# Kernel tuning notes

Hardware: AMD Instinct MI355X
Metric: run time of the kernel (lower is better)

The kernel has to match this reference:

```python
import jax, jax.numpy as jnp
import numpy as np

BATCH, IN_DIM, LATENT, K = 16384, 768, 12288, 32

def setup_inputs() -> dict:
    key = jax.random.key(0)
    k1, k2, k3 = jax.random.split(key, 3)
    # kaiming-uniform-style scale for encoder/decoder weights
    enc_bound = float(np.sqrt(6.0 / IN_DIM))
    dec_bound = float(np.sqrt(6.0 / LATENT))
    x = jax.random.normal(k1, (BATCH, IN_DIM), dtype=jnp.float32)
    enc_w = jax.random.uniform(k2, (LATENT, IN_DIM), dtype=jnp.float32, minval=-enc_bound, maxval=enc_bound)
    enc_b = jnp.zeros((LATENT,), dtype=jnp.float32)
    dec_w = jax.random.uniform(k3, (IN_DIM, LATENT), dtype=jnp.float32, minval=-dec_bound, maxval=dec_bound)
    dec_b = jnp.zeros((IN_DIM,), dtype=jnp.float32)
    return {"x": x, "enc_w": enc_w, "enc_b": enc_b, "dec_w": dec_w, "dec_b": dec_b, "k": K}

def reference(x, enc_w, enc_b, dec_w, dec_b, k):
    # encode: z = x @ W_e^T + b_e            [B, LATENT]
    z = jnp.einsum('bi,li->bl', x, enc_w) + enc_b
    # top-k threshold: kth largest value per row, then shifted relu
    vals, _ = jax.lax.top_k(z, k)
    thresh = vals[:, -1:]                     # [B, 1]
    z_sparse = jax.nn.relu(z - thresh)
    # decode: dense GEMM over all latent columns (as in original module)
    x_recon = jnp.einsum('bl,il->bi', z_sparse, dec_w) + dec_b
    return (x_recon, z_sparse)
```

## Files before the change

kernel.cpp:

```cpp
#include <hip/hip_runtime.h>

#define M_DIM 16384
#define K_DIM 768
#define N_DIM 12288
#define TOPK  32

typedef float f32x4 __attribute__((ext_vector_type(4)));
typedef short s16x8 __attribute__((ext_vector_type(8)));

__device__ __forceinline__ unsigned f2u(float f) {
  union { float f; unsigned u; } v; v.f = f; return v.u;
}
__device__ __forceinline__ float u2f(unsigned u) {
  union { unsigned u; float f; } v; v.u = u; return v.f;
}
__device__ __forceinline__ unsigned fkey(float f) {
  const unsigned u = f2u(f);
  return u ^ (unsigned)(((int)u >> 31) | 0x80000000);
}
__device__ __forceinline__ float kinv(unsigned k) {
  return u2f((k & 0x80000000u) ? (k ^ 0x80000000u) : ~k);
}

__device__ __forceinline__ unsigned short bf16_rne(float f) {
  unsigned u = f2u(f);
  return (unsigned short)((u + 0x7FFFu + ((u >> 16) & 1u)) >> 16);
}

__global__ __launch_bounds__(256) void split_bf16_planes(
    const float* __restrict__ src, unsigned short* __restrict__ hi,
    unsigned short* __restrict__ lo, int n4)
{
  const int stride = (int)(gridDim.x * blockDim.x);
  for (int i = (int)(blockIdx.x * blockDim.x + threadIdx.x); i < n4; i += stride) {
    const float4 v = ((const float4*)src)[i];
    ushort4 h, l;
    h.x = bf16_rne(v.x); h.y = bf16_rne(v.y); h.z = bf16_rne(v.z); h.w = bf16_rne(v.w);
    l.x = bf16_rne(v.x - u2f((unsigned)h.x << 16));
    l.y = bf16_rne(v.y - u2f((unsigned)h.y << 16));
    l.z = bf16_rne(v.z - u2f((unsigned)h.z << 16));
    l.w = bf16_rne(v.w - u2f((unsigned)h.w << 16));
    ((ushort4*)hi)[i] = h;
    ((ushort4*)lo)[i] = l;
  }
}

__device__ __forceinline__ void mfma16(f32x4& d, s16x8 a, s16x8 b) {
  asm("v_mfma_f32_16x16x32_bf16 %0, %1, %2, %0" : "+v"(d) : "v"(a), "v"(b));
}

#define GL16(g, l) __builtin_amdgcn_global_load_lds(                      \
    (const __attribute__((address_space(1))) void*)(g),                   \
    (__attribute__((address_space(3))) void*)(l), 16, 0, 0)

__global__ __launch_bounds__(256, 2) void TopKSparseAutoencoder_51917564674099_kernel(
    const unsigned short* __restrict__ Ahi, const unsigned short* __restrict__ Alo,
    const unsigned short* __restrict__ Bhi, const unsigned short* __restrict__ Blo,
    const float* __restrict__ bias, float* __restrict__ Z)
{
  __shared__ unsigned short lds[4][128][32];

  const int t    = (int)threadIdx.x;
  const int wid  = t >> 6;
  const int lane = t & 63;

  const int bid  = (int)(blockIdx.y * gridDim.x + blockIdx.x);
  const int bswz = (bid & 7) * (12288 / 8) + (bid >> 3);
  const int n0   = (bswz % 96) * 128;
  const int m0   = (bswz / 96) * 128;

  const int rr  = lane >> 2;
  const int kq  = lane & 3;
  const int rt0 = wid * 32 + rr;
  const int rt1 = rt0 + 16;
  const int kc0 = (kq ^ ((rt0 >> 1) & 3)) * 8;
  const int kc1 = (kq ^ ((rt1 >> 1) & 3)) * 8;
  const size_t offA0 = (size_t)(m0 + rt0) * K_DIM + kc0;
  const size_t offA1 = (size_t)(m0 + rt1) * K_DIM + kc1;
  const size_t offB0 = (size_t)(n0 + rt0) * K_DIM + kc0;
  const size_t offB1 = (size_t)(n0 + rt1) * K_DIM + kc1;

  const int wm = (wid >> 1) * 64;
  const int wn = (wid & 1) * 64;
  const int lr = lane & 15;
  const int lc = lane >> 4;

  f32x4 acc[4][4];
#pragma unroll
  for (int i = 0; i < 4; ++i)
#pragma unroll
    for (int j = 0; j < 4; ++j) acc[i][j] = (f32x4){0.f, 0.f, 0.f, 0.f};

  for (int k0 = 0; k0 < K_DIM; k0 += 32) {
    GL16(Ahi + offA0 + k0, &lds[0][wid * 32][0]);
    GL16(Ahi + offA1 + k0, &lds[0][wid * 32 + 16][0]);
    GL16(Alo + offA0 + k0, &lds[1][wid * 32][0]);
    GL16(Alo + offA1 + k0, &lds[1][wid * 32 + 16][0]);
    GL16(Bhi + offB0 + k0, &lds[2][wid * 32][0]);
    GL16(Bhi + offB1 + k0, &lds[2][wid * 32 + 16][0]);
    GL16(Blo + offB0 + k0, &lds[3][wid * 32][0]);
    GL16(Blo + offB1 + k0, &lds[3][wid * 32 + 16][0]);
    __syncthreads();

    s16x8 ah[4], al[4], bh[4], bl[4];
#pragma unroll
    for (int i = 0; i < 4; ++i) {
      const int r = wm + i * 16 + lr;
      const int p = (lc ^ ((r >> 1) & 3)) * 8;
      ah[i] = *(const s16x8*)&lds[0][r][p];
      al[i] = *(const s16x8*)&lds[1][r][p];
    }
#pragma unroll
    for (int j = 0; j < 4; ++j) {
      const int r = wn + j * 16 + lr;
      const int p = (lc ^ ((r >> 1) & 3)) * 8;
      bh[j] = *(const s16x8*)&lds[2][r][p];
      bl[j] = *(const s16x8*)&lds[3][r][p];
    }
#pragma unroll
    for (int i = 0; i < 4; ++i)
#pragma unroll
      for (int j = 0; j < 4; ++j) {
        mfma16(acc[i][j], ah[i], bh[j]);
        mfma16(acc[i][j], ah[i], bl[j]);
        mfma16(acc[i][j], al[i], bh[j]);
      }
    __syncthreads();
  }

  asm volatile("s_nop 7\n\ts_nop 7" :::);

#pragma unroll
  for (int j = 0; j < 4; ++j) {
    const int col = n0 + wn + j * 16 + lr;
    const float bb = bias[col];
#pragma unroll
    for (int i = 0; i < 4; ++i) {
      const int r0 = m0 + wm + i * 16 + lc * 4;
#pragma unroll
      for (int q = 0; q < 4; ++q)
        Z[(size_t)(r0 + q) * N_DIM + col] = acc[i][j][q] + bb;
    }
  }
}

__global__ void enc_gemm_f32_fb(
    const float* A, const float* B, const float* bias, float* Z)
{
  __shared__ float As[32][132];
  __shared__ float Bs[32][132];

  const int tx = (int)threadIdx.x;
  const int ty = (int)threadIdx.y;
  const int t  = ty * 16 + tx;
  const int n0 = (int)blockIdx.x * 128;
  const int m0 = (int)blockIdx.y * 128;
  const int r = t >> 1;
  const int h = (t & 1) * 16;

  float c[8][8];
#pragma unroll
  for (int i = 0; i < 8; ++i)
#pragma unroll
    for (int j = 0; j < 8; ++j) c[i][j] = 0.0f;

  for (int k0 = 0; k0 < K_DIM; k0 += 32) {
    const float* pa = A + (size_t)(m0 + r) * K_DIM + k0 + h;
    const float* pb = B + (size_t)(n0 + r) * K_DIM + k0 + h;
    float fa[16], fb[16];
#pragma unroll
    for (int j = 0; j < 16; ++j) fa[j] = pa[j];
#pragma unroll
    for (int j = 0; j < 16; ++j) fb[j] = pb[j];
#pragma unroll
    for (int j = 0; j < 16; ++j) As[h + j][r] = fa[j];
#pragma unroll
    for (int j = 0; j < 16; ++j) Bs[h + j][r] = fb[j];
    __syncthreads();

    for (int kk = 0; kk < 32; ++kk) {
      float av[8], bv[8];
#pragma unroll
      for (int i = 0; i < 8; ++i) av[i] = As[kk][ty * 8 + i];
#pragma unroll
      for (int j = 0; j < 8; ++j) bv[j] = Bs[kk][tx * 8 + j];
#pragma unroll
      for (int i = 0; i < 8; ++i)
#pragma unroll
        for (int j = 0; j < 8; ++j) c[i][j] += av[i] * bv[j];
    }
    __syncthreads();
  }

#pragma unroll
  for (int j = 0; j < 8; ++j) {
    const int col = n0 + tx * 8 + j;
    const float bb = bias[col];
#pragma unroll
    for (int i = 0; i < 8; ++i)
      Z[(size_t)(m0 + ty * 8 + i) * N_DIM + col] = c[i][j] + bb;
  }
}

__global__ void transpose_decw(const float* W, float* WT)
{
  __shared__ float tile[32][33];
  const int bx = (int)blockIdx.x;
  const int by = (int)blockIdx.y;
  const int tx = (int)threadIdx.x;
  const int ty = (int)threadIdx.y;
#pragma unroll
  for (int j = 0; j < 32; j += 8)
    tile[ty + j][tx] = W[(size_t)(by * 32 + ty + j) * N_DIM + bx * 32 + tx];
  __syncthreads();
#pragma unroll
  for (int j = 0; j < 32; j += 8)
    WT[(size_t)(bx * 32 + ty + j) * K_DIM + by * 32 + tx] = tile[tx][ty + j];
}

__device__ __forceinline__ void full_round(
    const uint4* zk, unsigned red[][2][4], int t, int lane, int wid, int r,
    unsigned& lo, unsigned long long& w)
{
  w >>= 2;
  const unsigned wu = (unsigned)w;
  const unsigned m1 = lo + wu, m2 = lo + 2u * wu, m3 = lo + 3u * wu;
  unsigned c1 = 0, c2 = 0, c3 = 0;
#pragma unroll
  for (int j = 0; j < 12; ++j) {
    const uint4 k = zk[t + 256 * j];
    c1 += (k.x >= m1) + (k.y >= m1) + (k.z >= m1) + (k.w >= m1);
    c2 += (k.x >= m2) + (k.y >= m2) + (k.z >= m2) + (k.w >= m2);
    c3 += (k.x >= m3) + (k.y >= m3) + (k.z >= m3) + (k.w >= m3);
  }
  unsigned p = c1 | (c2 << 16), q = c3;
  p += __shfl_down(p, 32); q += __shfl_down(q, 32);
  p += __shfl_down(p, 16); q += __shfl_down(q, 16);
  p += __shfl_down(p, 8);  q += __shfl_down(q, 8);
  p += __shfl_down(p, 4);  q += __shfl_down(q, 4);
  p += __shfl_down(p, 2);  q += __shfl_down(q, 2);
  p += __shfl_down(p, 1);  q += __shfl_down(q, 1);
  const int par = r & 1;
  if (lane == 0) { red[par][0][wid] = p; red[par][1][wid] = q; }
  __syncthreads();
  const unsigned P = red[par][0][0] + red[par][0][1] + red[par][0][2] + red[par][0][3];
  const unsigned Q = red[par][1][0] + red[par][1][1] + red[par][1][2] + red[par][1][3];
  if (Q >= (unsigned)TOPK)                lo = m3;
  else if ((P >> 16) >= (unsigned)TOPK)   lo = m2;
  else if ((P & 0xFFFFu) >= (unsigned)TOPK) lo = m1;
}

__global__ __launch_bounds__(256, 3) void topk_select_decode(
    float* Z,
    const float* __restrict__ WT,
    const float* __restrict__ DW,
    const float* __restrict__ db,
    float* __restrict__ XR,
    int use_wt)
{
  __shared__ uint4 zkey4[N_DIM / 4];
  __shared__ unsigned red[2][2][4];
  __shared__ unsigned cand[256];
  __shared__ unsigned s_T;
  __shared__ int s_cc;
  __shared__ int s_nnz;
  __shared__ int   s_col[TOPK];
  __shared__ float s_val[TOPK];

  const int row  = (int)blockIdx.x;
  const int t    = (int)threadIdx.x;
  const int lane = t & 63;
  const int wid  = t >> 6;

  float4* zv = (float4*)(Z + (size_t)row * N_DIM);

#pragma unroll
  for (int j = 0; j < 12; ++j) {
    const float4 v = zv[t + 256 * j];
    uint4 k;
    k.x = fkey(v.x); k.y = fkey(v.y); k.z = fkey(v.z); k.w = fkey(v.w);
    zkey4[t + 256 * j] = k;
  }
  if (t == 0) { s_nnz = 0; s_cc = 0; }
  if (t < TOPK) { s_col[t] = 0; s_val[t] = 0.0f; }
  __syncthreads();

  unsigned lo = 0;
  unsigned long long w = 1ULL << 32;
  for (int r = 0; r < 8; ++r)
    full_round(zkey4, red, t, lane, wid, r, lo, w);

#pragma unroll
  for (int j = 0; j < 12; ++j) {
    const uint4 k = zkey4[t + 256 * j];
    if (k.x >= lo) { int p = atomicAdd(&s_cc, 1); if (p < 256) cand[p] = k.x; }
    if (k.y >= lo) { int p = atomicAdd(&s_cc, 1); if (p < 256) cand[p] = k.y; }
    if (k.z >= lo) { int p = atomicAdd(&s_cc, 1); if (p < 256) cand[p] = k.z; }
    if (k.w >= lo) { int p = atomicAdd(&s_cc, 1); if (p < 256) cand[p] = k.w; }
  }
  __syncthreads();
  const int cc = s_cc;

  if (cc <= 256) {
    if (wid == 0) {
      const unsigned k0 = (lane       < cc) ? cand[lane]       : 0u;
      const unsigned k1 = (lane + 64  < cc) ? cand[lane + 64]  : 0u;
      const unsigned k2 = (lane + 128 < cc) ? cand[lane + 128] : 0u;
      const unsigned k3 = (lane + 192 < cc) ? cand[lane + 192] : 0u;
      for (int r = 8; r < 16; ++r) {
        w >>= 2;
        const unsigned wu = (unsigned)w;
        const unsigned m1 = lo + wu, m2 = lo + 2u * wu, m3 = lo + 3u * wu;
        unsigned c1 = (k0 >= m1) + (k1 >= m1) + (k2 >= m1) + (k3 >= m1);
        unsigned c2 = (k0 >= m2) + (k1 >= m2) + (k2 >= m2) + (k3 >= m2);
        unsigned c3 = (k0 >= m3) + (k1 >= m3) + (k2 >= m3) + (k3 >= m3);
        unsigned p = c1 | (c2 << 16), q = c3;
        p += __shfl_down(p, 32); q += __shfl_down(q, 32);
        p += __shfl_down(p, 16); q += __shfl_down(q, 16);
        p += __shfl_down(p, 8);  q += __shfl_down(q, 8);
        p += __shfl_down(p, 4);  q += __shfl_down(q, 4);
        p += __shfl_down(p, 2);  q += __shfl_down(q, 2);
        p += __shfl_down(p, 1);  q += __shfl_down(q, 1);
        p = __shfl(p, 0); q = __shfl(q, 0);
        if (q >= (unsigned)TOPK)                  lo = m3;
        else if ((p >> 16) >= (unsigned)TOPK)     lo = m2;
        else if ((p & 0xFFFFu) >= (unsigned)TOPK) lo = m1;
      }
      if (lane == 0) s_T = lo;
    }
  } else {
    for (int r = 8; r < 16; ++r)
      full_round(zkey4, red, t, lane, wid, r, lo, w);
    if (t == 0) s_T = lo;
  }
  __syncthreads();
  const unsigned T = s_T;
  const float thresh = kinv(T);

#define COMP(KF, OFS, OF) {                                                   \
      float v = 0.0f;                                                         \
      if (KF > T) {                                                           \
        v = kinv(KF) - thresh;                                                \
        const int p = atomicAdd(&s_nnz, 1);                                   \
        if (p < TOPK) { s_col[p] = base + OFS; s_val[p] = v; }                \
      }                                                                       \
      o.OF = v; }
#pragma unroll
  for (int j = 0; j < 12; ++j) {
    const uint4 k = zkey4[t + 256 * j];
    const int base = (t + 256 * j) * 4;
    float4 o;
    COMP(k.x, 0, x)
    COMP(k.y, 1, y)
    COMP(k.z, 2, z)
    COMP(k.w, 3, w)
    zv[t + 256 * j] = o;
  }
#undef COMP
  __syncthreads();

  float a0 = 0.0f, a1 = 0.0f, a2 = 0.0f;
  if (use_wt) {
#pragma unroll 8
    for (int j = 0; j < TOPK; ++j) {
      const float v = s_val[j];
      const float* wp = WT + (size_t)s_col[j] * K_DIM;
      a0 += v * wp[t];
      a1 += v * wp[t + 256];
      a2 += v * wp[t + 512];
    }
  } else {
#pragma unroll 8
    for (int j = 0; j < TOPK; ++j) {
      const float v = s_val[j];
      const int col = s_col[j];
      a0 += v * DW[(size_t)(t)       * N_DIM + col];
      a1 += v * DW[(size_t)(t + 256) * N_DIM + col];
      a2 += v * DW[(size_t)(t + 512) * N_DIM + col];
    }
  }
  float* xr = XR + (size_t)row * K_DIM;
  xr[t]       = a0 + db[t];
  xr[t + 256] = a1 + db[t + 256];
  xr[t + 512] = a2 + db[t + 512];
}

extern "C" void kernel_launch(void* const* d_in, const int* in_sizes, int n_in,
                              void* d_out, int out_size, void* d_ws, size_t ws_size,
                              hipStream_t stream)
{
  (void)in_sizes; (void)n_in; (void)out_size;

  const float* x     = (const float*)d_in[0];
  const float* enc_w = (const float*)d_in[1];
  const float* enc_b = (const float*)d_in[2];
  const float* dec_w = (const float*)d_in[3];
  const float* dec_b = (const float*)d_in[4];

  float* out     = (float*)d_out;
  float* x_recon = out;
  float* z_sp    = out + (size_t)M_DIM * K_DIM;

  const size_t WT_BYTES = (size_t)N_DIM * K_DIM * sizeof(float);
  const size_t XPLANE   = (size_t)M_DIM * K_DIM * sizeof(unsigned short);
  const size_t WPLANE   = (size_t)N_DIM * K_DIM * sizeof(unsigned short);
  const size_t FULL     = WT_BYTES + 2 * XPLANE + 2 * WPLANE;

  char* ws = (char*)d_ws;
  const int use_wt   = (ws_size >= WT_BYTES) ? 1 : 0;
  const int use_mfma = (ws_size >= FULL) ? 1 : 0;

  float*          WT  = (float*)ws;
  unsigned short* xhi = (unsigned short*)(ws + WT_BYTES);
  unsigned short* xlo = (unsigned short*)(ws + WT_BYTES + XPLANE);
  unsigned short* whi = (unsigned short*)(ws + WT_BYTES + 2 * XPLANE);
  unsigned short* wlo = (unsigned short*)(ws + WT_BYTES + 2 * XPLANE + WPLANE);

  if (use_wt) {
    dim3 tb(32, 8);
    dim3 tg(N_DIM / 32, K_DIM / 32);
    transpose_decw<<<tg, tb, 0, stream>>>(dec_w, WT);
  }

  if (use_mfma) {
    split_bf16_planes<<<1024, 256, 0, stream>>>(x, xhi, xlo, M_DIM * K_DIM / 4);
    split_bf16_planes<<<1024, 256, 0, stream>>>(enc_w, whi, wlo, N_DIM * K_DIM / 4);
    dim3 tg(N_DIM / 128, M_DIM / 128);
    TopKSparseAutoencoder_51917564674099_kernel<<<tg, 256, 0, stream>>>(
        xhi, xlo, whi, wlo, enc_b, z_sp);
  } else {
    dim3 tb(16, 16);
    dim3 tg(N_DIM / 128, M_DIM / 128);
    enc_gemm_f32_fb<<<tg, tb, 0, stream>>>(x, enc_w, enc_b, z_sp);
  }

  topk_select_decode<<<M_DIM, 256, 0, stream>>>(z_sp, WT, dec_w, dec_b, x_recon, use_wt);
}
```

Measured before the change: 2.410 ms.

## Emit per-chunk row maxima from encoder GEMM to prune top-k candidate search

The encoder GEMM epilogue now reduces each 128-column tile to per-row maxima and writes them to a workspace array. A new decode kernel first finds a lower bound from those 96 chunk maxima (the 32nd largest chunk max), gathers candidates above it into a small LDS list, and runs the radix select on that list instead of the full row. It also writes zeros with the other waves and scatters the sparse values back. The transpose and bf16 split kernels are merged into one prep launch. This is meant to cut the full-row select passes and launch overhead, at the cost of extra epilogue shuffles, an LDS barrier in the GEMM, and more workspace, which could disable the new path if the workspace is too small.

```diff
diff --git a/kernel.cpp b/kernel.cpp
--- a/kernel.cpp
+++ b/kernel.cpp
@@ -4,6 +4,7 @@
 #define K_DIM 768
 #define N_DIM 12288
 #define TOPK  32
+#define NCHUNK (N_DIM / 128)
 
 typedef float f32x4 __attribute__((ext_vector_type(4)));
 typedef short s16x8 __attribute__((ext_vector_type(8)));
@@ -21,18 +22,47 @@
 __device__ __forceinline__ float kinv(unsigned k) {
   return u2f((k & 0x80000000u) ? (k ^ 0x80000000u) : ~k);
 }
-
 __device__ __forceinline__ unsigned short bf16_rne(float f) {
   unsigned u = f2u(f);
   return (unsigned short)((u + 0x7FFFu + ((u >> 16) & 1u)) >> 16);
 }
 
-__global__ __launch_bounds__(256) void split_bf16_planes(
-    const float* __restrict__ src, unsigned short* __restrict__ hi,
-    unsigned short* __restrict__ lo, int n4)
+__global__ __launch_bounds__(256) void TopKSparseAutoencoder_51917564674099_prep(
+    const float* __restrict__ x, const float* __restrict__ w,
+    const float* __restrict__ dw,
+    unsigned short* __restrict__ xhi, unsigned short* __restrict__ xlo,
+    unsigned short* __restrict__ whi, unsigned short* __restrict__ wlo,
+    float* __restrict__ WT, int do_t, int do_s)
 {
-  const int stride = (int)(gridDim.x * blockDim.x);
-  for (int i = (int)(blockIdx.x * blockDim.x + threadIdx.x); i < n4; i += stride) {
+  __shared__ float tile[32][33];
+  const int b = (int)blockIdx.x;
+  const int t = (int)threadIdx.x;
+
+  if (b < 9216) {
+    if (!do_t) return;
+    const int bx = b % (N_DIM / 32);
+    const int by = b / (N_DIM / 32);
+    const int tx = t & 31, ty = t >> 5;
+#pragma unroll
+    for (int j = 0; j < 32; j += 8)
+      tile[ty + j][tx] = dw[(size_t)(by * 32 + ty + j) * N_DIM + bx * 32 + tx];
+    __syncthreads();
+#pragma unroll
+    for (int j = 0; j < 32; j += 8)
+      WT[(size_t)(bx * 32 + ty + j) * K_DIM + by * 32 + tx] = tile[tx][ty + j];
+    return;
+  }
+  if (!do_s) return;
+
+  const float* src; unsigned short* dh; unsigned short* dl; int i, stride, n4;
+  if (b < 9216 + 1024) {
+    src = x; dh = xhi; dl = xlo;
+    i = (b - 9216) * 256 + t; stride = 1024 * 256; n4 = M_DIM * K_DIM / 4;
+  } else {
+    src = w; dh = whi; dl = wlo;
+    i = (b - 10240) * 256 + t; stride = 512 * 256; n4 = N_DIM * K_DIM / 4;
+  }
+  for (; i < n4; i += stride) {
     const float4 v = ((const float4*)src)[i];
     ushort4 h, l;
     h.x = bf16_rne(v.x); h.y = bf16_rne(v.y); h.z = bf16_rne(v.z); h.w = bf16_rne(v.w);
@@ -40,8 +70,8 @@
     l.y = bf16_rne(v.y - u2f((unsigned)h.y << 16));
     l.z = bf16_rne(v.z - u2f((unsigned)h.z << 16));
     l.w = bf16_rne(v.w - u2f((unsigned)h.w << 16));
-    ((ushort4*)hi)[i] = h;
-    ((ushort4*)lo)[i] = l;
+    ((ushort4*)dh)[i] = h;
+    ((ushort4*)dl)[i] = l;
   }
 }
 
@@ -56,9 +86,11 @@
 __global__ __launch_bounds__(256, 2) void TopKSparseAutoencoder_51917564674099_kernel(
     const unsigned short* __restrict__ Ahi, const unsigned short* __restrict__ Alo,
     const unsigned short* __restrict__ Bhi, const unsigned short* __restrict__ Blo,
-    const float* __restrict__ bias, float* __restrict__ Z)
+    const float* __restrict__ bias, float* __restrict__ Z,
+    float* __restrict__ cmax, int do_cmax)
 {
   __shared__ unsigned short lds[4][128][32];
+  __shared__ float cmx[128][2];
 
   const int t    = (int)threadIdx.x;
   const int wid  = t >> 6;
@@ -130,6 +162,12 @@
 
   asm volatile("s_nop 7\n\ts_nop 7" :::);
 
+  float mx[4][4];
+#pragma unroll
+  for (int i = 0; i < 4; ++i)
+#pragma unroll
+    for (int q = 0; q < 4; ++q) mx[i][q] = -3.4e38f;
+
 #pragma unroll
   for (int j = 0; j < 4; ++j) {
     const int col = n0 + wn + j * 16 + lr;
@@ -138,9 +176,32 @@
     for (int i = 0; i < 4; ++i) {
       const int r0 = m0 + wm + i * 16 + lc * 4;
 #pragma unroll
-      for (int q = 0; q < 4; ++q)
-        Z[(size_t)(r0 + q) * N_DIM + col] = acc[i][j][q] + bb;
-    }
+      for (int q = 0; q < 4; ++q) {
+        const float val = acc[i][j][q] + bb;
+        Z[(size_t)(r0 + q) * N_DIM + col] = val;
+        mx[i][q] = fmaxf(mx[i][q], val);
+      }
+    }
+  }
+
+  if (do_cmax) {
+#pragma unroll
+    for (int s = 1; s < 16; s <<= 1)
+#pragma unroll
+      for (int i = 0; i < 4; ++i)
+#pragma unroll
+        for (int q = 0; q < 4; ++q)
+          mx[i][q] = fmaxf(mx[i][q], __shfl_xor(mx[i][q], s));
+    if (lr == 0) {
+#pragma unroll
+      for (int i = 0; i < 4; ++i)
+#pragma unroll
+        for (int q = 0; q < 4; ++q)
+          cmx[wm + i * 16 + lc * 4 + q][wid & 1] = mx[i][q];
+    }
+    __syncthreads();
+    if (t < 128)
+      cmax[(size_t)(m0 + t) * NCHUNK + (n0 >> 7)] = fmaxf(cmx[t][0], cmx[t][1]);
   }
 }
 
@@ -202,23 +263,179 @@
   }
 }
 
-__global__ void transpose_decw(const float* W, float* WT)
+__global__ __launch_bounds__(256, 4) void TopKSparseAutoencoder_51917564674099_zdecode(
+    float* Z, const float* __restrict__ CMAX, const float* __restrict__ WT,
+    const float* __restrict__ db, float* __restrict__ XR)
 {
-  __shared__ float tile[32][33];
-  const int bx = (int)blockIdx.x;
-  const int by = (int)blockIdx.y;
-  const int tx = (int)threadIdx.x;
-  const int ty = (int)threadIdx.y;
-#pragma unroll
-  for (int j = 0; j < 32; j += 8)
-    tile[ty + j][tx] = W[(size_t)(by * 32 + ty + j) * N_DIM + bx * 32 + tx];
+  __shared__ unsigned candk[512];
+  __shared__ int      candi[512];
+  __shared__ unsigned red[2][2][4];
+  __shared__ unsigned s_B;
+  __shared__ int s_cc, s_nnz;
+  __shared__ int   s_col[TOPK];
+  __shared__ float s_val[TOPK];
+
+  const int row  = (int)blockIdx.x;
+  const int t    = (int)threadIdx.x;
+  const int lane = t & 63;
+  const int wid  = t >> 6;
+
+  if (t == 0) { s_cc = 0; s_nnz = 0; }
+  if (t < TOPK) { s_col[t] = 0; s_val[t] = 0.0f; }
+
+  if (wid == 0) {
+    const unsigned kA = fkey(CMAX[(size_t)row * NCHUNK + lane]);
+    const unsigned kB = (lane < NCHUNK - 64) ? fkey(CMAX[(size_t)row * NCHUNK + 64 + lane]) : 0u;
+    unsigned lo = 0;
+    unsigned long long w = 1ULL << 32;
+    for (int r = 0; r < 8; ++r) {
+      w >>= 2;
+      const unsigned wu = (unsigned)w;
+      const unsigned m1 = lo + wu, m2 = lo + 2u * wu, m3 = lo + 3u * wu;
+      unsigned p = (unsigned)((kA >= m1) + (kB >= m1)) |
+                   ((unsigned)((kA >= m2) + (kB >= m2)) << 16);
+      unsigned q = (unsigned)((kA >= m3) + (kB >= m3));
+      p += __shfl_down(p, 32); q += __shfl_down(q, 32);
+      p += __shfl_down(p, 16); q += __shfl_down(q, 16);
+      p += __shfl_down(p, 8);  q += __shfl_down(q, 8);
+      p += __shfl_down(p, 4);  q += __shfl_down(q, 4);
+      p += __shfl_down(p, 2);  q += __shfl_down(q, 2);
+      p += __shfl_down(p, 1);  q += __shfl_down(q, 1);
+      p = __shfl(p, 0); q = __shfl(q, 0);
+      if (q >= (unsigned)TOPK)                  lo = m3;
+      else if ((p >> 16) >= (unsigned)TOPK)     lo = m2;
+      else if ((p & 0xFFFFu) >= (unsigned)TOPK) lo = m1;
+    }
+    if (lane == 0) s_B = lo;
+  }
   __syncthreads();
-#pragma unroll
-  for (int j = 0; j < 32; j += 8)
-    WT[(size_t)(bx * 32 + ty + j) * K_DIM + by * 32 + tx] = tile[tx][ty + j];
-}
-
-__device__ __forceinline__ void full_round(
+  const unsigned B = s_B;
+
+  const float4* zr = (const float4*)(Z + (size_t)row * N_DIM);
+#pragma unroll
+  for (int j = 0; j < 12; ++j) {
+    const float4 v = zr[t + 256 * j];
+    const int base = (t + 256 * j) * 4;
+    const unsigned k0 = fkey(v.x), k1 = fkey(v.y), k2 = fkey(v.z), k3 = fkey(v.w);
+    if (k0 >= B) { int p = atomicAdd(&s_cc, 1); if (p < 512) { candk[p] = k0; candi[p] = base; } }
+    if (k1 >= B) { int p = atomicAdd(&s_cc, 1); if (p < 512) { candk[p] = k1; candi[p] = base + 1; } }
+    if (k2 >= B) { int p = atomicAdd(&s_cc, 1); if (p < 512) { candk[p] = k2; candi[p] = base + 2; } }
+    if (k3 >= B) { int p = atomicAdd(&s_cc, 1); if (p < 512) { candk[p] = k3; candi[p] = base + 3; } }
+  }
+  __syncthreads();
+  const int cc = s_cc;
+  float4* zw = (float4*)(Z + (size_t)row * N_DIM);
+
+  if (cc <= 512) {
+    if (wid == 0) {
+      unsigned k[8];
+#pragma unroll
+      for (int i = 0; i < 8; ++i) k[i] = (lane + 64 * i < cc) ? candk[lane + 64 * i] : 0u;
+      unsigned lo = 0;
+      unsigned long long w = 1ULL << 32;
+      for (int r = 0; r < 16; ++r) {
+        w >>= 2;
+        const unsigned wu = (unsigned)w;
+        const unsigned m1 = lo + wu, m2 = lo + 2u * wu, m3 = lo + 3u * wu;
+        unsigned c1 = 0, c2 = 0, c3 = 0;
+#pragma unroll
+        for (int i = 0; i < 8; ++i) {
+          c1 += (k[i] >= m1); c2 += (k[i] >= m2); c3 += (k[i] >= m3);
+        }
+        unsigned p = c1 | (c2 << 16), q = c3;
+        p += __shfl_down(p, 32); q += __shfl_down(q, 32);
+        p += __shfl_down(p, 16); q += __shfl_down(q, 16);
+        p += __shfl_down(p, 8);  q += __shfl_down(q, 8);
+        p += __shfl_down(p, 4);  q += __shfl_down(q, 4);
+        p += __shfl_down(p, 2);  q += __shfl_down(q, 2);
+        p += __shfl_down(p, 1);  q += __shfl_down(q, 1);
+        p = __shfl(p, 0); q = __shfl(q, 0);
+        if (q >= (unsigned)TOPK)                  lo = m3;
+        else if ((p >> 16) >= (unsigned)TOPK)     lo = m2;
+        else if ((p & 0xFFFFu) >= (unsigned)TOPK) lo = m1;
+      }
+      const unsigned T = lo;
+      const float thresh = kinv(T);
+      for (int i = lane; i < cc; i += 64) {
+        const unsigned ck = candk[i];
+        if (ck > T) {
+          const int p = atomicAdd(&s_nnz, 1);
+          if (p < TOPK) { s_col[p] = candi[i]; s_val[p] = kinv(ck) - thresh; }
+        }
+      }
+    } else {
+      const float4 z4 = {0.f, 0.f, 0.f, 0.f};
+#pragma unroll
+      for (int jj = 0; jj < 16; ++jj)
+        zw[(wid - 1) * 64 + lane + 192 * jj] = z4;
+    }
+    __syncthreads();
+  } else {
+    unsigned lo = 0;
+    unsigned long long w = 1ULL << 32;
+    for (int r = 0; r < 16; ++r) {
+      w >>= 2;
+      const unsigned wu = (unsigned)w;
+      const unsigned m1 = lo + wu, m2 = lo + 2u * wu, m3 = lo + 3u * wu;
+      unsigned c1 = 0, c2 = 0, c3 = 0;
+      for (int j = 0; j < 12; ++j) {
+        const float4 v = zr[t + 256 * j];
+        const unsigned k0 = fkey(v.x), k1 = fkey(v.y), k2 = fkey(v.z), k3 = fkey(v.w);
+        c1 += (k0 >= m1) + (k1 >= m1) + (k2 >= m1) + (k3 >= m1);
+        c2 += (k0 >= m2) + (k1 >= m2) + (k2 >= m2) + (k3 >= m2);
+        c3 += (k0 >= m3) + (k1 >= m3) + (k2 >= m3) + (k3 >= m3);
+      }
+      unsigned p = c1 | (c2 << 16), q = c3;
+      p += __shfl_down(p, 32); q += __shfl_down(q, 32);
+      p += __shfl_down(p, 16); q += __shfl_down(q, 16);
+      p += __shfl_down(p, 8);  q += __shfl_down(q, 8);
+      p += __shfl_down(p, 4);  q += __shfl_down(q, 4);
+      p += __shfl_down(p, 2);  q += __shfl_down(q, 2);
+      p += __shfl_down(p, 1);  q += __shfl_down(q, 1);
+      const int par = r & 1;
+      if (lane == 0) { red[par][0][wid] = p; red[par][1][wid] = q; }
+      __syncthreads();
+      const unsigned P = red[par][0][0] + red[par][0][1] + red[par][0][2] + red[par][0][3];
+      const unsigned Q = red[par][1][0] + red[par][1][1] + red[par][1][2] + red[par][1][3];
+      if (Q >= (unsigned)TOPK)                  lo = m3;
+      else if ((P >> 16) >= (unsigned)TOPK)     lo = m2;
+      else if ((P & 0xFFFFu) >= (unsigned)TOPK) lo = m1;
+    }
+    const unsigned T = lo;
+    const float thresh = kinv(T);
+    const float4 z4 = {0.f, 0.f, 0.f, 0.f};
+    for (int j = 0; j < 12; ++j) {
+      const float4 v = zr[t + 256 * j];
+      const int base = (t + 256 * j) * 4;
+      const unsigned k0 = fkey(v.x), k1 = fkey(v.y), k2 = fkey(v.z), k3 = fkey(v.w);
+      if (k0 > T) { int p = atomicAdd(&s_nnz, 1); if (p < TOPK) { s_col[p] = base;     s_val[p] = kinv(k0) - thresh; } }
+      if (k1 > T) { int p = atomicAdd(&s_nnz, 1); if (p < TOPK) { s_col[p] = base + 1; s_val[p] = kinv(k1) - thresh; } }
+      if (k2 > T) { int p = atomicAdd(&s_nnz, 1); if (p < TOPK) { s_col[p] = base + 2; s_val[p] = kinv(k2) - thresh; } }
+      if (k3 > T) { int p = atomicAdd(&s_nnz, 1); if (p < TOPK) { s_col[p] = base + 3; s_val[p] = kinv(k3) - thresh; } }
+      zw[t + 256 * j] = z4;
+    }
+    __syncthreads();
+  }
+
+  const int nnz = (s_nnz < TOPK) ? s_nnz : TOPK;
+  if (t < nnz) Z[(size_t)row * N_DIM + s_col[t]] = s_val[t];
+
+  float a0 = 0.0f, a1 = 0.0f, a2 = 0.0f;
+#pragma unroll 8
+  for (int j = 0; j < TOPK; ++j) {
+    const float v = s_val[j];
+    const float* wp = WT + (size_t)s_col[j] * K_DIM;
+    a0 += v * wp[t];
+    a1 += v * wp[t + 256];
+    a2 += v * wp[t + 512];
+  }
+  float* xr = XR + (size_t)row * K_DIM;
+  xr[t]       = a0 + db[t];
+  xr[t + 256] = a1 + db[t + 256];
+  xr[t + 512] = a2 + db[t + 512];
+}
+
+__device__ __forceinline__ void full_round_l(
     const uint4* zk, unsigned red[][2][4], int t, int lane, int wid, int r,
     unsigned& lo, unsigned long long& w)
 {
@@ -250,13 +467,9 @@
   else if ((P & 0xFFFFu) >= (unsigned)TOPK) lo = m1;
 }
 
-__global__ __launch_bounds__(256, 3) void topk_select_decode(
-    float* Z,
-    const float* __restrict__ WT,
-    const float* __restrict__ DW,
-    const float* __restrict__ db,
-    float* __restrict__ XR,
-    int use_wt)
+__global__ __launch_bounds__(256, 3) void topk_select_decode_fb(
+    float* Z, const float* __restrict__ WT, const float* __restrict__ DW,
+    const float* __restrict__ db, float* __restrict__ XR, int use_wt)
 {
   __shared__ uint4 zkey4[N_DIM / 4];
   __shared__ unsigned red[2][2][4];
@@ -288,7 +501,7 @@
   unsigned lo = 0;
   unsigned long long w = 1ULL << 32;
   for (int r = 0; r < 8; ++r)
-    full_round(zkey4, red, t, lane, wid, r, lo, w);
+    full_round_l(zkey4, red, t, lane, wid, r, lo, w);
 
 #pragma unroll
   for (int j = 0; j < 12; ++j) {
@@ -330,14 +543,14 @@
     }
   } else {
     for (int r = 8; r < 16; ++r)
-      full_round(zkey4, red, t, lane, wid, r, lo, w);
+      full_round_l(zkey4, red, t, lane, wid, r, lo, w);
     if (t == 0) s_T = lo;
   }
   __syncthreads();
   const unsigned T = s_T;
   const float thresh = kinv(T);
 
-#define COMP(KF, OFS, OF) {                                                   \
+#define COMPF(KF, OFS, OF) {                                                  \
       float v = 0.0f;                                                         \
       if (KF > T) {                                                           \
         v = kinv(KF) - thresh;                                                \
@@ -350,13 +563,13 @@
     const uint4 k = zkey4[t + 256 * j];
     const int base = (t + 256 * j) * 4;
     float4 o;
-    COMP(k.x, 0, x)
-    COMP(k.y, 1, y)
-    COMP(k.z, 2, z)
-    COMP(k.w, 3, w)
+    COMPF(k.x, 0, x)
+    COMPF(k.y, 1, y)
+    COMPF(k.z, 2, z)
+    COMPF(k.w, 3, w)
     zv[t + 256 * j] = o;
   }
-#undef COMP
+#undef COMPF
   __syncthreads();
 
   float a0 = 0.0f, a1 = 0.0f, a2 = 0.0f;
@@ -405,34 +618,39 @@
   const size_t XPLANE   = (size_t)M_DIM * K_DIM * sizeof(unsigned short);
   const size_t WPLANE   = (size_t)N_DIM * K_DIM * sizeof(unsigned short);
   const size_t FULL     = WT_BYTES + 2 * XPLANE + 2 * WPLANE;
+  const size_t CMAX_B   = (size_t)M_DIM * NCHUNK * sizeof(float);
+  const size_t FULL2    = FULL + CMAX_B;
 
   char* ws = (char*)d_ws;
   const int use_wt   = (ws_size >= WT_BYTES) ? 1 : 0;
   const int use_mfma = (ws_size >= FULL) ? 1 : 0;
-
-  float*          WT  = (float*)ws;
-  unsigned short* xhi = (unsigned short*)(ws + WT_BYTES);
-  unsigned short* xlo = (unsigned short*)(ws + WT_BYTES + XPLANE);
-  unsigned short* whi = (unsigned short*)(ws + WT_BYTES + 2 * XPLANE);
-  unsigned short* wlo = (unsigned short*)(ws + WT_BYTES + 2 * XPLANE + WPLANE);
-
-  if (use_wt) {
-    dim3 tb(32, 8);
-    dim3 tg(N_DIM / 32, K_DIM / 32);
-    transpose_decw<<<tg, tb, 0, stream>>>(dec_w, WT);
-  }
+  const int use_cmax = (ws_size >= FULL2) ? 1 : 0;
+
+  float*          WT   = (float*)ws;
+  unsigned short* xhi  = (unsigned short*)(ws + WT_BYTES);
+  unsigned short* xlo  = (unsigned short*)(ws + WT_BYTES + XPLANE);
+  unsigned short* whi  = (unsigned short*)(ws + WT_BYTES + 2 * XPLANE);
+  unsigned short* wlo  = (unsigned short*)(ws + WT_BYTES + 2 * XPLANE + WPLANE);
+  float*          CMAX = (float*)(ws + FULL);
+
+  if (use_wt || use_mfma)
+    TopKSparseAutoencoder_51917564674099_prep<<<10752, 256, 0, stream>>>(
+        x, enc_w, dec_w, xhi, xlo, whi, wlo, WT, use_wt, use_mfma);
 
   if (use_mfma) {
-    split_bf16_planes<<<1024, 256, 0, stream>>>(x, xhi, xlo, M_DIM * K_DIM / 4);
-    split_bf16_planes<<<1024, 256, 0, stream>>>(enc_w, whi, wlo, N_DIM * K_DIM / 4);
     dim3 tg(N_DIM / 128, M_DIM / 128);
     TopKSparseAutoencoder_51917564674099_kernel<<<tg, 256, 0, stream>>>(
-        xhi, xlo, whi, wlo, enc_b, z_sp);
+        xhi, xlo, whi, wlo, enc_b, z_sp, CMAX, use_cmax);
   } else {
     dim3 tb(16, 16);
     dim3 tg(N_DIM / 128, M_DIM / 128);
     enc_gemm_f32_fb<<<tg, tb, 0, stream>>>(x, enc_w, enc_b, z_sp);
   }
 
-  topk_select_decode<<<M_DIM, 256, 0, stream>>>(z_sp, WT, dec_w, dec_b, x_recon, use_wt);
-}
+  if (use_cmax)
+    TopKSparseAutoencoder_51917564674099_zdecode<<<M_DIM, 256, 0, stream>>>(
+        z_sp, CMAX, WT, dec_b, x_recon);
+  else
+    topk_select_decode_fb<<<M_DIM, 256, 0, stream>>>(
+        z_sp, WT, dec_w, dec_b, x_recon, use_wt);
+}
```

Result: faster. 2.232 ms (-7.4%).
